# Optimization experiments

Measured on AMD Instinct MI355X. Metric: run time of the kernel, lower is better.

The kernel has to match this reference:

```python
import jax, jax.numpy as jnp
from jax import lax
import numpy as np

VOCAB, TAGS, EMBED, HIDDEN, BATCH, SEQ = 50000, 9, 300, 1000, 32, 200


def setup_inputs() -> dict:
    key = jax.random.key(0)
    ks = jax.random.split(key, 12)
    s_e = 1.0 / np.sqrt(HIDDEN)
    inp = {
        "x": jax.random.randint(ks[0], (SEQ, BATCH), 0, VOCAB),
        "y": jax.random.randint(ks[1], (SEQ, BATCH), 0, TAGS),
        "embed_w": jax.random.normal(ks[2], (VOCAB, EMBED), jnp.float32),
        "W_ih": jax.random.uniform(ks[3], (4 * HIDDEN, EMBED), jnp.float32, -s_e, s_e),
        "W_hh": jax.random.uniform(ks[4], (4 * HIDDEN, HIDDEN), jnp.float32, -s_e, s_e),
        "b_ih": jax.random.uniform(ks[5], (4 * HIDDEN,), jnp.float32, -s_e, s_e),
        "b_hh": jax.random.uniform(ks[6], (4 * HIDDEN,), jnp.float32, -s_e, s_e),
        "lin_w": jax.random.uniform(ks[7], (TAGS, HIDDEN), jnp.float32, -s_e, s_e),
        "lin_b": jax.random.uniform(ks[8], (TAGS,), jnp.float32, -s_e, s_e),
        "start_trans": jax.random.uniform(ks[9], (TAGS,), jnp.float32, -0.1, 0.1),
        "end_trans": jax.random.uniform(ks[10], (TAGS,), jnp.float32, -0.1, 0.1),
        "trans": jax.random.uniform(ks[11], (TAGS, TAGS), jnp.float32, -0.1, 0.1),
    }
    return inp


def _forward(x, y, embed_w, W_ih, W_hh, b_ih, b_hh, lin_w, lin_b, start_trans, end_trans, trans):
    T, B = x.shape
    H = W_hh.shape[1]
    embeds = embed_w[x]  # [T,B,E]
    # Precompute input contribution to gates: [T,B,4H]
    xg = jnp.einsum("tbe,ge->tbg", embeds, W_ih) + b_ih + b_hh

    def lstm_step(carry, xg_t):
        h, c = carry
        g = xg_t + h @ W_hh.T  # [B,4H]
        i, f, gg, o = jnp.split(g, 4, axis=-1)  # PyTorch gate order i,f,g,o
        c = jax.nn.sigmoid(f) * c + jax.nn.sigmoid(i) * jnp.tanh(gg)
        h = jax.nn.sigmoid(o) * jnp.tanh(c)
        return (h, c), h

    h0 = jnp.zeros((B, H), embeds.dtype)
    _, hs = lax.scan(lstm_step, (h0, h0), xg)  # hs: [T,B,H]

    tag_space = jnp.einsum("tbh,kh->tbk", hs, lin_w) + lin_b  # [T,B,K]
    # Faithful to original: log_softmax over dim=1 (the batch axis)
    emissions = jax.nn.log_softmax(tag_space, axis=1)

    # ---- CRF log-likelihood (pytorch-crf semantics, full mask, sum reduction) ----
    b_idx = jnp.arange(B)
    em_at_y = jnp.take_along_axis(emissions, y[:, :, None], axis=2)[:, :, 0]  # [T,B]
    numerator = (
        start_trans[y[0]]
        + em_at_y.sum(axis=0)
        + trans[y[:-1], y[1:]].sum(axis=0)
        + end_trans[y[-1]]
    )  # [B]

    alpha0 = start_trans[None, :] + emissions[0]  # [B,K]

    def crf_step(alpha, em_t):
        # alpha: [B,K] over previous tag; em_t: [B,K]
        nxt = jax.nn.logsumexp(alpha[:, :, None] + trans[None, :, :] + em_t[:, None, :], axis=1)
        return nxt, None

    alpha, _ = lax.scan(crf_step, alpha0, emissions[1:])
    log_z = jax.nn.logsumexp(alpha + end_trans[None, :], axis=1)  # [B]
    return (numerator - log_z).sum()


def reference(x, y, embed_w, W_ih, W_hh, b_ih, b_hh, lin_w, lin_b, start_trans, end_trans, trans):
    return _forward(x, y, embed_w, W_ih, W_hh, b_ih, b_hh, lin_w, lin_b, start_trans, end_trans, trans)
```

## Files before the change

kernel.cpp:

```cpp
#include <hip/hip_runtime.h>

#define T_SEQ 200
#define NB    32
#define NE    300
#define NH    1000
#define NK    9
#define NJ    4096
#define EPD   320
#define WSCALE 256.0f
#define HSCALE 16.0f
#define LSCALE 512.0f
#define GSCALE (1.0f / (256.0f * 16.0f))
#define TSCALE (1.0f / (16.0f * 512.0f))

typedef __attribute__((ext_vector_type(4))) float f32x4;
typedef __attribute__((ext_vector_type(8))) short s16x8;
typedef __attribute__((ext_vector_type(4))) short s16x4;
typedef unsigned long long u64;

__device__ __forceinline__ unsigned short f2bf(float f) {
    union { float f; unsigned u; } v; v.f = f;
    unsigned r = v.u + 0x7FFFu + ((v.u >> 16) & 1u);
    return (unsigned short)(r >> 16);
}
__device__ __forceinline__ float bf2f(unsigned short h) {
    union { unsigned u; float f; } v; v.u = ((unsigned)h) << 16;
    return v.f;
}
__device__ __forceinline__ float ftanh(float x) {
    float e = __expf(fminf(2.f * x, 80.f));
    return (e - 1.f) / (e + 1.f);
}
__device__ __forceinline__ float fsig(float x) {
    return 1.f / (1.f + __expf(-x));
}
__device__ __forceinline__ unsigned nt_poll(const unsigned* p) {
    unsigned r;
    asm volatile("global_load_dword %0, %1, off nt\n\t"
                 "s_waitcnt vmcnt(0)"
                 : "=v"(r) : "v"(p) : "memory");
    return r;
}
__device__ __forceinline__ void plain_pub(unsigned* p, unsigned v) {
    __hip_atomic_store(p, v, __ATOMIC_RELAXED, __HIP_MEMORY_SCOPE_WORKGROUP);
}

__global__ __launch_bounds__(256) void prep_emb(
    const int* __restrict__ x, const float* __restrict__ embed_w,
    unsigned short* __restrict__ emb_bf, unsigned* __restrict__ ctrl)
{
    const int t = blockIdx.x, tid = threadIdx.x;
    if (blockIdx.x == 0) {
        for (int i = tid; i < 2048; i += 256)
            ctrl[i] = (i == 497) ? 0xffffffffu : 0u;
    }
    for (int idx = tid; idx < NB * EPD; idx += 256) {
        int b = idx / EPD, e = idx - b * EPD;
        float v = (e < NE) ? embed_w[(size_t)x[t * NB + b] * NE + e] : 0.f;
        emb_bf[((size_t)t * NB + b) * EPD + e] = f2bf(v);
    }
}

__global__ __launch_bounds__(256) void prep_w(
    const float* __restrict__ W_ih, const float* __restrict__ b_ih,
    const float* __restrict__ b_hh, const float* __restrict__ lin_w,
    unsigned short* __restrict__ wih_bf, float* __restrict__ biasg,
    unsigned char* __restrict__ linw_q)
{
    const int blk = blockIdx.x, tid = threadIdx.x;
    for (int idx = tid; idx < 64 * EPD; idx += 256) {
        int jr = idx / EPD, e = idx - jr * EPD;
        int jp = blk * 64 + jr;
        int wgu = jp >> 7, rr = jp & 127, g = rr >> 5, uu = rr & 31;
        int m = wgu * 32 + uu;
        float v = (m < NH && e < NE) ? W_ih[(size_t)(g * NH + m) * NE + e] : 0.f;
        wih_bf[(size_t)jp * EPD + e] = f2bf(v);
    }
    if (tid < 64) {
        int jp = blk * 64 + tid;
        int wgu = jp >> 7, rr = jp & 127, g = rr >> 5, uu = rr & 31;
        int m = wgu * 32 + uu;
        biasg[jp] = (m < NH) ? (b_ih[g * NH + m] + b_hh[g * NH + m]) : 0.f;
    }
    if (blk < 16) {
        int n = blk, k = tid * 4;
        float v0 = (n < NK && k + 0 < NH) ? lin_w[(size_t)n * NH + k + 0] * LSCALE : 0.f;
        float v1 = (n < NK && k + 1 < NH) ? lin_w[(size_t)n * NH + k + 1] * LSCALE : 0.f;
        float v2 = (n < NK && k + 2 < NH) ? lin_w[(size_t)n * NH + k + 2] * LSCALE : 0.f;
        float v3 = (n < NK && k + 3 < NH) ? lin_w[(size_t)n * NH + k + 3] * LSCALE : 0.f;
        int p01 = __builtin_amdgcn_cvt_pk_fp8_f32(v0, v1, 0, false);
        int p23 = __builtin_amdgcn_cvt_pk_fp8_f32(v2, v3, 0, false);
        ((unsigned*)linw_q)[n * 256 + tid] =
            ((unsigned)p01 & 0xffffu) | ((unsigned)p23 << 16);
    }
}

__device__ __forceinline__ int gate_xg(unsigned* done, int ready, int tn, int lane) {
    while (ready <= tn) {
        unsigned v = 64u;
        if (lane < 8 && ready + lane < T_SEQ)
            v = __hip_atomic_load(&done[ready + lane], __ATOMIC_RELAXED,
                                  __HIP_MEMORY_SCOPE_AGENT);
        unsigned m = (unsigned)__ballot((int)(v >= 64u)) & 255u;
        if (m & 1u) {
            unsigned run = (m == 255u) ? 8u : (unsigned)__builtin_ctz(~m);
            ready += (int)run;
        } else {
            __builtin_amdgcn_s_sleep(1);
        }
    }
    return ready;
}

__global__ __launch_bounds__(256, 1) void lstm_kernel(
    const float* __restrict__ W_hh,
    const unsigned short* __restrict__ emb_bf,
    const unsigned short* __restrict__ wih_bf,
    const float* __restrict__ biasg,
    unsigned short* __restrict__ xg,
    unsigned char* __restrict__ h_q,
    unsigned* __restrict__ ctrl)
{
    __shared__ __align__(16) unsigned char s_w[128 * 1024];
    __shared__ int s_chunk, s_grp, s_pid, s_mode;

    const int tid = threadIdx.x;

    if (tid == 0) {
        unsigned xcc;
        asm volatile("s_getreg_b32 %0, hwreg(HW_REG_XCC_ID)" : "=s"(xcc));
        xcc &= 15u;
        unsigned myidx = __hip_atomic_fetch_add(&ctrl[480 + xcc], 1u,
                             __ATOMIC_RELAXED, __HIP_MEMORY_SCOPE_AGENT);
        __threadfence();
        unsigned tot = __hip_atomic_fetch_add(&ctrl[496], 1u,
                             __ATOMIC_RELAXED, __HIP_MEMORY_SCOPE_AGENT);
        if (tot == 255u) {
            __threadfence();
            unsigned w0 = 0xffu, w1 = 0xffu;
            for (unsigned xx = 0; xx < 16; ++xx) {
                unsigned cx = __hip_atomic_load(&ctrl[480 + xx], __ATOMIC_RELAXED,
                                                __HIP_MEMORY_SCOPE_AGENT);
                if (cx >= 32u) {
                    if (w0 == 0xffu) w0 = xx;
                    else { w1 = xx; break; }
                }
            }
            __hip_atomic_store(&ctrl[497], w0 | (w1 << 8), __ATOMIC_RELAXED,
                               __HIP_MEMORY_SCOPE_AGENT);
        }
        unsigned win;
        do {
            win = __hip_atomic_load(&ctrl[497], __ATOMIC_RELAXED,
                                    __HIP_MEMORY_SCOPE_AGENT);
        } while (win == 0xffffffffu);
        unsigned w0 = win & 0xffu, w1 = (win >> 8) & 0xffu;
        int grp = -1;
        if (xcc == w0 && myidx < 32u) grp = 0;
        else if (xcc == w1 && myidx < 32u) grp = 1;
        s_grp = grp;
        s_chunk = (grp >= 0) ? (int)myidx : -1;
        s_pid = (grp >= 0) ? -1
                     : (int)__hip_atomic_fetch_add(&ctrl[498], 1u,
                           __ATOMIC_RELAXED, __HIP_MEMORY_SCOPE_AGENT);
    }
    __syncthreads();
    const int chunk = s_chunk;
    const int w = tid >> 6, lane = tid & 63;
    const int col = lane & 15, quad = lane >> 4;
    unsigned* done = ctrl + 256;

    if (chunk < 0) {
        const int pid = s_pid;
        for (int g = pid; g < T_SEQ * 64; g += 192) {
            const int t = g >> 6, jt = g & 63;
            const unsigned short* eb = emb_bf + (size_t)t * NB * EPD;
            const unsigned short* wb = wih_bf + (size_t)(jt * 64 + w * 16 + col) * EPD;
            const unsigned short* ea0 = eb + (size_t)col * EPD;
            const unsigned short* ea1 = eb + (size_t)(16 + col) * EPD;

            f32x4 acc0 = {0.f, 0.f, 0.f, 0.f};
            f32x4 acc1 = {0.f, 0.f, 0.f, 0.f};
#pragma unroll
            for (int kc = 0; kc < EPD / 32; ++kc) {
                int ko = kc * 32 + quad * 8;
                s16x8 a0 = *(const s16x8*)&ea0[ko];
                s16x8 a1 = *(const s16x8*)&ea1[ko];
                s16x8 bb = *(const s16x8*)&wb[ko];
                acc0 = __builtin_amdgcn_mfma_f32_16x16x32_bf16(a0, bb, acc0, 0, 0, 0);
                acc1 = __builtin_amdgcn_mfma_f32_16x16x32_bf16(a1, bb, acc1, 0, 0, 0);
            }
            const int jp = jt * 64 + w * 16 + col;
            const float bi = biasg[jp];
            size_t base = ((size_t)t * NJ + jp) * NB;
            union { s16x4 v; u64 q; } p0, p1;
#pragma unroll
            for (int r = 0; r < 4; ++r) {
                p0.v[r] = (short)f2bf(acc0[r] + bi);
                p1.v[r] = (short)f2bf(acc1[r] + bi);
            }
            __hip_atomic_store((u64*)&xg[base + quad * 4], p0.q,
                               __ATOMIC_RELAXED, __HIP_MEMORY_SCOPE_AGENT);
            __hip_atomic_store((u64*)&xg[base + 16 + quad * 4], p1.q,
                               __ATOMIC_RELAXED, __HIP_MEMORY_SCOPE_AGENT);
            __syncthreads();
            if (tid == 0)
                __hip_atomic_fetch_add(&done[t], 1u, __ATOMIC_RELAXED,
                                       __HIP_MEMORY_SCOPE_AGENT);
        }
        return;
    }

    const int grp = s_grp;
    const size_t GOFF = (size_t)grp * 16384;
    unsigned* slowf = ctrl + grp * 64;
    unsigned* fastf = ctrl + 128 + grp * 64;
    unsigned* s_w32 = (unsigned*)s_w;

    for (int idx = tid; idx < 128 * 256; idx += 256) {
        int r = idx >> 8, dw = idx & 255;
        int g = r >> 5, uu = r & 31, m = chunk * 32 + uu;
        float4 w4 = make_float4(0.f, 0.f, 0.f, 0.f);
        if (m < NH && dw < 250)
            w4 = *(const float4*)&W_hh[(size_t)(g * NH + m) * NH + dw * 4];
        int p0 = __builtin_amdgcn_cvt_pk_fp8_f32(w4.x * WSCALE, w4.y * WSCALE, 0, false);
        int p1 = __builtin_amdgcn_cvt_pk_fp8_f32(w4.z * WSCALE, w4.w * WSCALE, 0, false);
        unsigned v = ((unsigned)p0 & 0xffffu) | ((unsigned)p1 << 16);
        int kb = dw >> 1;
        int kbs = kb ^ (r & 15);
        s_w32[r * 256 + (kbs << 1) + (dw & 1)] = v;
    }
    if (tid < 128)
        *(unsigned*)(h_q + GOFF + (size_t)chunk * 512 + tid * 4) = 0u;
    __syncthreads();
    if (tid == 0) {
        plain_pub(&fastf[chunk * 2 + 0], 1u);
        plain_pub(&fastf[chunk * 2 + 1], 1u);
        __hip_atomic_store(&slowf[chunk * 2 + 0], 1u, __ATOMIC_RELAXED,
                           __HIP_MEMORY_SCOPE_AGENT);
        __hip_atomic_store(&slowf[chunk * 2 + 1], 1u, __ATOMIC_RELAXED,
                           __HIP_MEMORY_SCOPE_AGENT);
    }
    if (grp == 0 && chunk == 0 && w == 0) {
        int md = 2;
        for (int it = 0; it < 8192; ++it) {
            unsigned v = nt_poll(&fastf[lane]);
            if (__all((int)(v >= 1u))) { md = 1; break; }
        }
        if (lane == 0) {
            __hip_atomic_store(&ctrl[499], (unsigned)md, __ATOMIC_RELAXED,
                               __HIP_MEMORY_SCOPE_AGENT);
            s_mode = md;
        }
    } else if (tid == 0) {
        unsigned m;
        do {
            m = __hip_atomic_load(&ctrl[499], __ATOMIC_RELAXED,
                                  __HIP_MEMORY_SCOPE_AGENT);
        } while (m == 0u);
        s_mode = (int)m;
    }
    __syncthreads();
    const int mode = s_mode;

    if (w >= 2) return;
    const int p = w;
    const int fid = chunk * 2 + w;

    int ready = gate_xg(done, 0, 1, lane);
    s16x4 xcur[4], xnxt[4];
#pragma unroll
    for (int g = 0; g < 4; ++g)
        xcur[g] = *(const s16x4*)&xg[((size_t)0 * NJ + chunk * 128 + (2 * g + p) * 16 + col) * NB
                                     + grp * 16 + quad * 4];

    float c[4] = {0.f, 0.f, 0.f, 0.f};
    const int rw = quad * 4;
    const int boff = col * 32 + quad * 8;

    for (int t = 0; t < T_SEQ; ++t) {
        const unsigned need = (unsigned)(t + 1);
        const int gt = t + 2;
        bool gate_pending = (gt < T_SEQ) && (ready <= gt);
        if (mode == 1) {
            for (;;) {
                unsigned v = nt_poll(&fastf[lane]);
                bool hok = __all((int)(v >= need));
                if (gate_pending) {
                    unsigned d = 64u;
                    if (lane < 8 && ready + lane < T_SEQ)
                        d = __hip_atomic_load(&done[ready + lane], __ATOMIC_RELAXED,
                                              __HIP_MEMORY_SCOPE_AGENT);
                    unsigned m = (unsigned)__ballot((int)(d >= 64u)) & 255u;
                    if (m & 1u)
                        ready += (m == 255u) ? 8 : (int)__builtin_ctz(~m);
                    gate_pending = (ready <= gt);
                }
                if (hok && !gate_pending) break;
            }
        } else {
            for (;;) {
                unsigned v = __hip_atomic_load(&slowf[lane], __ATOMIC_RELAXED,
                                               __HIP_MEMORY_SCOPE_AGENT);
                bool hok = __all((int)(v >= need));
                if (gate_pending) {
                    unsigned d = 64u;
                    if (lane < 8 && ready + lane < T_SEQ)
                        d = __hip_atomic_load(&done[ready + lane], __ATOMIC_RELAXED,
                                              __HIP_MEMORY_SCOPE_AGENT);
                    unsigned m = (unsigned)__ballot((int)(d >= 64u)) & 255u;
                    if (m & 1u)
                        ready += (m == 255u) ? 8 : (int)__builtin_ctz(~m);
                    gate_pending = (ready <= gt);
                }
                if (hok && !gate_pending) break;
            }
        }
        asm volatile("" ::: "memory");

        const unsigned char* pb = h_q + (size_t)t * 32768 + GOFF + boff;
        u64 a[32];
#pragma unroll
        for (int kc = 0; kc < 32; ++kc)
            a[kc] = *(const u64*)(pb + (size_t)kc * 512);

        if (t + 1 < T_SEQ) {
#pragma unroll
            for (int g = 0; g < 4; ++g)
                xnxt[g] = *(const s16x4*)&xg[((size_t)(t + 1) * NJ + chunk * 128 + (2 * g + p) * 16 + col) * NB
                                             + grp * 16 + quad * 4];
        }

        f32x4 acc0 = {0.f, 0.f, 0.f, 0.f};
        f32x4 acc1 = {0.f, 0.f, 0.f, 0.f};
        f32x4 acc2 = {0.f, 0.f, 0.f, 0.f};
        f32x4 acc3 = {0.f, 0.f, 0.f, 0.f};
#pragma unroll
        for (int kc = 0; kc < 32; ++kc) {
            int kb = kc * 4 + quad;
            u64 b0 = *(const u64*)&s_w[((0 * 2 + p) * 16 + col) * 1024 + ((kb ^ col) << 3)];
            u64 b1 = *(const u64*)&s_w[((1 * 2 + p) * 16 + col) * 1024 + ((kb ^ col) << 3)];
            u64 b2 = *(const u64*)&s_w[((2 * 2 + p) * 16 + col) * 1024 + ((kb ^ col) << 3)];
            u64 b3 = *(const u64*)&s_w[((3 * 2 + p) * 16 + col) * 1024 + ((kb ^ col) << 3)];
            acc0 = __builtin_amdgcn_mfma_f32_16x16x32_fp8_fp8((long)a[kc], (long)b0, acc0, 0, 0, 0);
            acc1 = __builtin_amdgcn_mfma_f32_16x16x32_fp8_fp8((long)a[kc], (long)b1, acc1, 0, 0, 0);
            acc2 = __builtin_amdgcn_mfma_f32_16x16x32_fp8_fp8((long)a[kc], (long)b2, acc2, 0, 0, 0);
            acc3 = __builtin_amdgcn_mfma_f32_16x16x32_fp8_fp8((long)a[kc], (long)b3, acc3, 0, 0, 0);
        }

        float hv[4];
#pragma unroll
        for (int r = 0; r < 4; ++r) {
            float gi = acc0[r] * GSCALE + bf2f((unsigned short)xcur[0][r]);
            float gf = acc1[r] * GSCALE + bf2f((unsigned short)xcur[1][r]);
            float gg = acc2[r] * GSCALE + bf2f((unsigned short)xcur[2][r]);
            float go = acc3[r] * GSCALE + bf2f((unsigned short)xcur[3][r]);
            c[r] = fsig(gf) * c[r] + fsig(gi) * ftanh(gg);
            hv[r] = fsig(go) * ftanh(c[r]);
        }
        {
            int p01 = __builtin_amdgcn_cvt_pk_fp8_f32(hv[0] * HSCALE, hv[1] * HSCALE, 0, false);
            int p23 = __builtin_amdgcn_cvt_pk_fp8_f32(hv[2] * HSCALE, hv[3] * HSCALE, 0, false);
            unsigned char* pg = h_q + (size_t)(t + 1) * 32768 + GOFF + (size_t)chunk * 512
                              + p * 16 + col;
            pg[(rw + 0) * 32] = (unsigned char)(p01 & 0xff);
            pg[(rw + 1) * 32] = (unsigned char)((p01 >> 8) & 0xff);
            pg[(rw + 2) * 32] = (unsigned char)(p23 & 0xff);
            pg[(rw + 3) * 32] = (unsigned char)((p23 >> 8) & 0xff);
        }
        asm volatile("s_waitcnt vmcnt(0)" ::: "memory");
        if (lane == 0) {
            plain_pub(&fastf[fid], (unsigned)(t + 2));
            if (mode == 2)
                __hip_atomic_store(&slowf[fid], (unsigned)(t + 2),
                                   __ATOMIC_RELAXED, __HIP_MEMORY_SCOPE_AGENT);
        }
#pragma unroll
        for (int g = 0; g < 4; ++g) xcur[g] = xnxt[g];
    }
}

__global__ __launch_bounds__(128) void tagem_kernel(
    const unsigned char* __restrict__ h_q,
    const unsigned char* __restrict__ linw_q,
    const float* __restrict__ lin_b,
    float* __restrict__ em)
{
    __shared__ float s_ts[NB * NK];
    __shared__ float s_lse[NK];
    const int t = blockIdx.x, tid = threadIdx.x;
    const int w = tid >> 6, lane = tid & 63;
    const int col = lane & 15, quad = lane >> 4;
    const unsigned char* pa = h_q + (size_t)(t + 1) * 32768 + (size_t)w * 16384
                            + col * 32 + quad * 8;
    const unsigned char* pw = linw_q + (size_t)col * 1024 + quad * 8;

    f32x4 acc = {0.f, 0.f, 0.f, 0.f};
#pragma unroll 8
    for (int kc = 0; kc < 32; ++kc) {
        u64 a  = *(const u64*)(pa + (size_t)kc * 512);
        u64 bv = *(const u64*)(pw + kc * 32);
        acc = __builtin_amdgcn_mfma_f32_16x16x32_fp8_fp8((long)a, (long)bv, acc, 0, 0, 0);
    }
    if (col < NK) {
        float lb = lin_b[col];
#pragma unroll
        for (int r = 0; r < 4; ++r)
            s_ts[(w * 16 + quad * 4 + r) * NK + col] = acc[r] * TSCALE + lb;
    }
    __syncthreads();
    if (tid < NK) {
        float m = -1e30f;
        for (int bb = 0; bb < NB; ++bb) m = fmaxf(m, s_ts[bb * NK + tid]);
        float s = 0.f;
        for (int bb = 0; bb < NB; ++bb) s += __expf(s_ts[bb * NK + tid] - m);
        s_lse[tid] = m + __logf(s);
    }
    __syncthreads();
    for (int idx = tid; idx < NB * NK; idx += 128) {
        int k = idx - (idx / NK) * NK;
        em[(size_t)t * NB * NK + idx] = s_ts[idx] - s_lse[k];
    }
}

__global__ __launch_bounds__(512) void crf_kernel(
    const int* __restrict__ y, const float* __restrict__ em,
    const float* __restrict__ start_trans, const float* __restrict__ end_trans,
    const float* __restrict__ trans, float* __restrict__ out)
{
    __shared__ float s_trans[NK * NK];
    __shared__ float s_red[NB];
    __shared__ int   s_y[T_SEQ * NB];
    const int tid = threadIdx.x;
    const int gb = tid >> 4;
    const int q  = tid & 15;
    const int lane = tid & 63;
    const int gbase = lane & 48;

    if (tid < NK * NK) s_trans[tid] = trans[tid];
    for (int i = tid; i < T_SEQ * NB; i += 512) s_y[i] = y[i];
    __syncthreads();

    float trC[NK];
#pragma unroll
    for (int i = 0; i < NK; ++i)
        trC[i] = (q < NK) ? s_trans[i * NK + q] : 0.f;

    float emv0 = (q < NK) ? em[gb * NK + q] : -1e30f;
    int yp = s_y[gb];
    float num = start_trans[yp] + __shfl(emv0, gbase | yp, 64);
    float alpha = (q < NK) ? (start_trans[q] + emv0) : -1e30f;

    float e[8];
#pragma unroll
    for (int j = 0; j < 8; ++j) {
        int t = 1 + j;
        e[j] = (q < NK && t < T_SEQ) ? em[(size_t)(t * NB + gb) * NK + q] : -1e30f;
    }
    for (int blk = 0; blk < 25; ++blk) {
        float enx[8];
        const int tb = 1 + (blk + 1) * 8;
#pragma unroll
        for (int j = 0; j < 8; ++j) {
            int t = tb + j;
            enx[j] = (q < NK && t < T_SEQ) ? em[(size_t)(t * NB + gb) * NK + q] : -1e30f;
        }
#pragma unroll
        for (int j = 0; j < 8; ++j) {
            int t = 1 + blk * 8 + j;
            if (t < T_SEQ) {
                float ev = e[j];
                int yc = s_y[t * NB + gb];
                num += s_trans[yp * NK + yc] + __shfl(ev, gbase | yc, 64);
                yp = yc;
                float a_i[NK];
#pragma unroll
                for (int i = 0; i < NK; ++i)
                    a_i[i] = __shfl(alpha, gbase | i, 64) + trC[i];
                float m = a_i[0];
#pragma unroll
                for (int i = 1; i < NK; ++i) m = fmaxf(m, a_i[i]);
                float s = 0.f;
#pragma unroll
                for (int i = 0; i < NK; ++i) s += __expf(a_i[i] - m);
                alpha = (q < NK) ? (ev + m + __logf(s)) : -1e30f;
            }
        }
#pragma unroll
        for (int j = 0; j < 8; ++j) e[j] = enx[j];
    }

    num += end_trans[yp];
    float v = (q < NK) ? (alpha + end_trans[q]) : -1e30f;
    float mg = v;
#pragma unroll
    for (int off = 8; off >= 1; off >>= 1)
        mg = fmaxf(mg, __shfl_xor(mg, off, 64));
    float sg = __expf(v - mg);
#pragma unroll
    for (int off = 8; off >= 1; off >>= 1)
        sg += __shfl_xor(sg, off, 64);
    float lz = mg + __logf(sg);
    if (q == 0) s_red[gb] = num - lz;
    __syncthreads();
    if (tid == 0) {
        float tot = 0.f;
        for (int i = 0; i < NB; ++i) tot += s_red[i];
        out[0] = tot;
    }
}

extern "C" void kernel_launch(void* const* d_in, const int* in_sizes, int n_in,
                              void* d_out, int out_size, void* d_ws, size_t ws_size,
                              hipStream_t stream)
{
    const int*   x           = (const int*)d_in[0];
    const int*   y           = (const int*)d_in[1];
    const float* embed_w     = (const float*)d_in[2];
    const float* W_ih        = (const float*)d_in[3];
    const float* W_hh        = (const float*)d_in[4];
    const float* b_ih        = (const float*)d_in[5];
    const float* b_hh        = (const float*)d_in[6];
    const float* lin_w       = (const float*)d_in[7];
    const float* lin_b       = (const float*)d_in[8];
    const float* start_trans = (const float*)d_in[9];
    const float* end_trans   = (const float*)d_in[10];
    const float* trans       = (const float*)d_in[11];
    float* out = (float*)d_out;

    char* ws = (char*)d_ws;
    unsigned short* xg     = (unsigned short*)(ws);
    unsigned char*  h_q    = (unsigned char*)(ws + 52428800);
    unsigned char*  linw_q = (unsigned char*)(ws + 59015168);
    float*          em     = (float*)(ws + 65601536);
    unsigned*       ctrl   = (unsigned*)(ws + 65831936);
    float*          biasg  = (float*)(ws + 65840128);
    unsigned short* emb_bf = (unsigned short*)(ws + 65856512);
    unsigned short* wih_bf = (unsigned short*)(ws + 69952512);

    prep_emb<<<dim3(T_SEQ), 256, 0, stream>>>(x, embed_w, emb_bf, ctrl);
    prep_w<<<dim3(64), 256, 0, stream>>>(W_ih, b_ih, b_hh, lin_w, wih_bf, biasg, linw_q);

    lstm_kernel<<<dim3(256), 256, 0, stream>>>(W_hh, emb_bf, wih_bf, biasg,
                                               xg, h_q, ctrl);

    tagem_kernel<<<dim3(T_SEQ), 128, 0, stream>>>(h_q, linw_q, lin_b, em);
    crf_kernel<<<dim3(1), 512, 0, stream>>>(y, em, start_trans, end_trans, trans, out);
}
```

Measured before the change: 983.5 us.

## Offload flag polling to helper waves and merge prep kernels

Two otherwise idle waves per workgroup now do all global polling. One tracks the per-chunk h-ready flags, the other tracks the xg-done counters, and each relays progress through shared-memory variables that the two compute waves spin on. This takes global-memory polling latency off the recurrent critical path. The next-step xg load now happens after the h store and before the publish, and the publish waits with a partial vmcnt. The two prep kernels are also fused into one launch. The risks are the looser waitcnt ordering between the stores and the flag publish, and extra wave activity on the CU.

```diff
diff --git a/kernel.cpp b/kernel.cpp
--- a/kernel.cpp
+++ b/kernel.cpp
@@ -45,45 +45,45 @@
     __hip_atomic_store(p, v, __ATOMIC_RELAXED, __HIP_MEMORY_SCOPE_WORKGROUP);
 }
 
-__global__ __launch_bounds__(256) void prep_emb(
+__global__ __launch_bounds__(256) void prep_all(
     const int* __restrict__ x, const float* __restrict__ embed_w,
-    unsigned short* __restrict__ emb_bf, unsigned* __restrict__ ctrl)
-{
-    const int t = blockIdx.x, tid = threadIdx.x;
-    if (blockIdx.x == 0) {
-        for (int i = tid; i < 2048; i += 256)
-            ctrl[i] = (i == 497) ? 0xffffffffu : 0u;
-    }
-    for (int idx = tid; idx < NB * EPD; idx += 256) {
-        int b = idx / EPD, e = idx - b * EPD;
-        float v = (e < NE) ? embed_w[(size_t)x[t * NB + b] * NE + e] : 0.f;
-        emb_bf[((size_t)t * NB + b) * EPD + e] = f2bf(v);
-    }
-}
-
-__global__ __launch_bounds__(256) void prep_w(
     const float* __restrict__ W_ih, const float* __restrict__ b_ih,
     const float* __restrict__ b_hh, const float* __restrict__ lin_w,
-    unsigned short* __restrict__ wih_bf, float* __restrict__ biasg,
-    unsigned char* __restrict__ linw_q)
+    unsigned short* __restrict__ emb_bf, unsigned short* __restrict__ wih_bf,
+    float* __restrict__ biasg, unsigned char* __restrict__ linw_q,
+    unsigned* __restrict__ ctrl)
 {
     const int blk = blockIdx.x, tid = threadIdx.x;
+    if (blk < T_SEQ) {
+        const int t = blk;
+        if (blk == 0) {
+            for (int i = tid; i < 2048; i += 256)
+                ctrl[i] = (i == 497) ? 0xffffffffu : 0u;
+        }
+        for (int idx = tid; idx < NB * EPD; idx += 256) {
+            int b = idx / EPD, e = idx - b * EPD;
+            float v = (e < NE) ? embed_w[(size_t)x[t * NB + b] * NE + e] : 0.f;
+            emb_bf[((size_t)t * NB + b) * EPD + e] = f2bf(v);
+        }
+        return;
+    }
+    const int b2 = blk - T_SEQ;
     for (int idx = tid; idx < 64 * EPD; idx += 256) {
         int jr = idx / EPD, e = idx - jr * EPD;
-        int jp = blk * 64 + jr;
+        int jp = b2 * 64 + jr;
         int wgu = jp >> 7, rr = jp & 127, g = rr >> 5, uu = rr & 31;
         int m = wgu * 32 + uu;
         float v = (m < NH && e < NE) ? W_ih[(size_t)(g * NH + m) * NE + e] : 0.f;
         wih_bf[(size_t)jp * EPD + e] = f2bf(v);
     }
     if (tid < 64) {
-        int jp = blk * 64 + tid;
+        int jp = b2 * 64 + tid;
         int wgu = jp >> 7, rr = jp & 127, g = rr >> 5, uu = rr & 31;
         int m = wgu * 32 + uu;
         biasg[jp] = (m < NH) ? (b_ih[g * NH + m] + b_hh[g * NH + m]) : 0.f;
     }
-    if (blk < 16) {
-        int n = blk, k = tid * 4;
+    if (b2 < 16) {
+        int n = b2, k = tid * 4;
         float v0 = (n < NK && k + 0 < NH) ? lin_w[(size_t)n * NH + k + 0] * LSCALE : 0.f;
         float v1 = (n < NK && k + 1 < NH) ? lin_w[(size_t)n * NH + k + 1] * LSCALE : 0.f;
         float v2 = (n < NK && k + 2 < NH) ? lin_w[(size_t)n * NH + k + 2] * LSCALE : 0.f;
@@ -93,23 +93,6 @@
         ((unsigned*)linw_q)[n * 256 + tid] =
             ((unsigned)p01 & 0xffffu) | ((unsigned)p23 << 16);
     }
-}
-
-__device__ __forceinline__ int gate_xg(unsigned* done, int ready, int tn, int lane) {
-    while (ready <= tn) {
-        unsigned v = 64u;
-        if (lane < 8 && ready + lane < T_SEQ)
-            v = __hip_atomic_load(&done[ready + lane], __ATOMIC_RELAXED,
-                                  __HIP_MEMORY_SCOPE_AGENT);
-        unsigned m = (unsigned)__ballot((int)(v >= 64u)) & 255u;
-        if (m & 1u) {
-            unsigned run = (m == 255u) ? 8u : (unsigned)__builtin_ctz(~m);
-            ready += (int)run;
-        } else {
-            __builtin_amdgcn_s_sleep(1);
-        }
-    }
-    return ready;
 }
 
 __global__ __launch_bounds__(256, 1) void lstm_kernel(
@@ -123,10 +106,12 @@
 {
     __shared__ __align__(16) unsigned char s_w[128 * 1024];
     __shared__ int s_chunk, s_grp, s_pid, s_mode;
+    __shared__ int s_go, s_ready;
 
     const int tid = threadIdx.x;
 
     if (tid == 0) {
+        s_go = 0; s_ready = 0;
         unsigned xcc;
         asm volatile("s_getreg_b32 %0, hwreg(HW_REG_XCC_ID)" : "=s"(xcc));
         xcc &= 15u;
@@ -263,59 +248,58 @@
     __syncthreads();
     const int mode = s_mode;
 
-    if (w >= 2) return;
+    volatile int* vgo = (volatile int*)&s_go;
+    volatile int* vready = (volatile int*)&s_ready;
+
+    if (w == 2) {
+        int need = 1;
+        while (need <= T_SEQ) {
+            unsigned v;
+            if (mode == 1) v = nt_poll(&fastf[lane]);
+            else v = __hip_atomic_load(&slowf[lane], __ATOMIC_RELAXED,
+                                       __HIP_MEMORY_SCOPE_AGENT);
+            while (need <= T_SEQ && __all((int)(v >= (unsigned)need))) {
+                if (lane == 0) *vgo = need;
+                ++need;
+            }
+        }
+        return;
+    }
+    if (w == 3) {
+        int ready = 0;
+        while (ready < T_SEQ) {
+            unsigned v = 64u;
+            if (lane < 8 && ready + lane < T_SEQ)
+                v = __hip_atomic_load(&done[ready + lane], __ATOMIC_RELAXED,
+                                      __HIP_MEMORY_SCOPE_AGENT);
+            unsigned m = (unsigned)__ballot((int)(v >= 64u)) & 255u;
+            if (m & 1u) {
+                ready += (m == 255u) ? 8 : (int)__builtin_ctz(~m);
+                if (lane == 0) *vready = ready;
+            } else {
+                __builtin_amdgcn_s_sleep(1);
+            }
+        }
+        return;
+    }
+
     const int p = w;
     const int fid = chunk * 2 + w;
 
-    int ready = gate_xg(done, 0, 1, lane);
-    s16x4 xcur[4], xnxt[4];
+    while (*vready < 1) { }
+    asm volatile("" ::: "memory");
+    s16x4 xA[4], xB[4];
 #pragma unroll
     for (int g = 0; g < 4; ++g)
-        xcur[g] = *(const s16x4*)&xg[((size_t)0 * NJ + chunk * 128 + (2 * g + p) * 16 + col) * NB
-                                     + grp * 16 + quad * 4];
+        xA[g] = *(const s16x4*)&xg[((size_t)0 * NJ + chunk * 128 + (2 * g + p) * 16 + col) * NB
+                                   + grp * 16 + quad * 4];
 
     float c[4] = {0.f, 0.f, 0.f, 0.f};
     const int rw = quad * 4;
     const int boff = col * 32 + quad * 8;
 
-    for (int t = 0; t < T_SEQ; ++t) {
-        const unsigned need = (unsigned)(t + 1);
-        const int gt = t + 2;
-        bool gate_pending = (gt < T_SEQ) && (ready <= gt);
-        if (mode == 1) {
-            for (;;) {
-                unsigned v = nt_poll(&fastf[lane]);
-                bool hok = __all((int)(v >= need));
-                if (gate_pending) {
-                    unsigned d = 64u;
-                    if (lane < 8 && ready + lane < T_SEQ)
-                        d = __hip_atomic_load(&done[ready + lane], __ATOMIC_RELAXED,
-                                              __HIP_MEMORY_SCOPE_AGENT);
-                    unsigned m = (unsigned)__ballot((int)(d >= 64u)) & 255u;
-                    if (m & 1u)
-                        ready += (m == 255u) ? 8 : (int)__builtin_ctz(~m);
-                    gate_pending = (ready <= gt);
-                }
-                if (hok && !gate_pending) break;
-            }
-        } else {
-            for (;;) {
-                unsigned v = __hip_atomic_load(&slowf[lane], __ATOMIC_RELAXED,
-                                               __HIP_MEMORY_SCOPE_AGENT);
-                bool hok = __all((int)(v >= need));
-                if (gate_pending) {
-                    unsigned d = 64u;
-                    if (lane < 8 && ready + lane < T_SEQ)
-                        d = __hip_atomic_load(&done[ready + lane], __ATOMIC_RELAXED,
-                                              __HIP_MEMORY_SCOPE_AGENT);
-                    unsigned m = (unsigned)__ballot((int)(d >= 64u)) & 255u;
-                    if (m & 1u)
-                        ready += (m == 255u) ? 8 : (int)__builtin_ctz(~m);
-                    gate_pending = (ready <= gt);
-                }
-                if (hok && !gate_pending) break;
-            }
-        }
+    auto step = [&](int t, s16x4 (&xin)[4], s16x4 (&xout)[4]) {
+        while (*vgo < t + 1) { }
         asm volatile("" ::: "memory");
 
         const unsigned char* pb = h_q + (size_t)t * 32768 + GOFF + boff;
@@ -323,13 +307,6 @@
 #pragma unroll
         for (int kc = 0; kc < 32; ++kc)
             a[kc] = *(const u64*)(pb + (size_t)kc * 512);
-
-        if (t + 1 < T_SEQ) {
-#pragma unroll
-            for (int g = 0; g < 4; ++g)
-                xnxt[g] = *(const s16x4*)&xg[((size_t)(t + 1) * NJ + chunk * 128 + (2 * g + p) * 16 + col) * NB
-                                             + grp * 16 + quad * 4];
-        }
 
         f32x4 acc0 = {0.f, 0.f, 0.f, 0.f};
         f32x4 acc1 = {0.f, 0.f, 0.f, 0.f};
@@ -351,10 +328,10 @@
         float hv[4];
 #pragma unroll
         for (int r = 0; r < 4; ++r) {
-            float gi = acc0[r] * GSCALE + bf2f((unsigned short)xcur[0][r]);
-            float gf = acc1[r] * GSCALE + bf2f((unsigned short)xcur[1][r]);
-            float gg = acc2[r] * GSCALE + bf2f((unsigned short)xcur[2][r]);
-            float go = acc3[r] * GSCALE + bf2f((unsigned short)xcur[3][r]);
+            float gi = acc0[r] * GSCALE + bf2f((unsigned short)xin[0][r]);
+            float gf = acc1[r] * GSCALE + bf2f((unsigned short)xin[1][r]);
+            float gg = acc2[r] * GSCALE + bf2f((unsigned short)xin[2][r]);
+            float go = acc3[r] * GSCALE + bf2f((unsigned short)xin[3][r]);
             c[r] = fsig(gf) * c[r] + fsig(gi) * ftanh(gg);
             hv[r] = fsig(go) * ftanh(c[r]);
         }
@@ -368,15 +345,29 @@
             pg[(rw + 2) * 32] = (unsigned char)(p23 & 0xff);
             pg[(rw + 3) * 32] = (unsigned char)((p23 >> 8) & 0xff);
         }
-        asm volatile("s_waitcnt vmcnt(0)" ::: "memory");
-        if (lane == 0) {
-            plain_pub(&fastf[fid], (unsigned)(t + 2));
-            if (mode == 2)
-                __hip_atomic_store(&slowf[fid], (unsigned)(t + 2),
-                                   __ATOMIC_RELAXED, __HIP_MEMORY_SCOPE_AGENT);
-        }
-#pragma unroll
-        for (int g = 0; g < 4; ++g) xcur[g] = xnxt[g];
+        asm volatile("" ::: "memory");
+
+        if (t + 1 < T_SEQ) {
+            while (*vready < t + 2) { }
+            asm volatile("" ::: "memory");
+#pragma unroll
+            for (int g = 0; g < 4; ++g)
+                xout[g] = *(const s16x4*)&xg[((size_t)(t + 1) * NJ + chunk * 128 + (2 * g + p) * 16 + col) * NB
+                                             + grp * 16 + quad * 4];
+            asm volatile("" ::: "memory");
+            asm volatile("s_waitcnt vmcnt(4)" ::: "memory");
+            if (lane == 0) {
+                plain_pub(&fastf[fid], (unsigned)(t + 2));
+                if (mode == 2)
+                    __hip_atomic_store(&slowf[fid], (unsigned)(t + 2),
+                                       __ATOMIC_RELAXED, __HIP_MEMORY_SCOPE_AGENT);
+            }
+        }
+    };
+
+    for (int tt = 0; tt < T_SEQ; tt += 2) {
+        step(tt + 0, xA, xB);
+        step(tt + 1, xB, xA);
     }
 }
 
@@ -538,8 +529,9 @@
     unsigned short* emb_bf = (unsigned short*)(ws + 65856512);
     unsigned short* wih_bf = (unsigned short*)(ws + 69952512);
 
-    prep_emb<<<dim3(T_SEQ), 256, 0, stream>>>(x, embed_w, emb_bf, ctrl);
-    prep_w<<<dim3(64), 256, 0, stream>>>(W_ih, b_ih, b_hh, lin_w, wih_bf, biasg, linw_q);
+    prep_all<<<dim3(T_SEQ + 64), 256, 0, stream>>>(x, embed_w, W_ih, b_ih, b_hh,
+                                                   lin_w, emb_bf, wih_bf, biasg,
+                                                   linw_q, ctrl);
 
     lstm_kernel<<<dim3(256), 256, 0, stream>>>(W_hh, emb_bf, wih_bf, biasg,
                                                xg, h_q, ctrl);
```

After: 1.290 ms. 31.2% more time.

## Merge prep kernels, fuse tag emission with CRF via flags, relax LSTM publish wait

Applied to the files above, without the earlier changes.

Combines the two prep kernels into one launch, and merges the tag-emission and CRF kernels into a single grid. In the merged grid the CRF block polls per-timestep flags so it can start consuming emissions while other blocks are still producing them. In the LSTM loop, the next step's xg prefetch is now issued before the h-publish flag, and the wait before publishing is vmcnt(4) instead of vmcnt(0), so the prefetch loads stay in flight. The loop is also unrolled by two with ping-pong buffers. The changes aim to cut launch overhead and shorten the critical path of the recurrence. The risk is that the CRF block spin-waits if it is scheduled before the producer blocks, and that the relaxed wait count depends on the exact order of outstanding memory operations.

```diff
diff --git a/kernel.cpp b/kernel.cpp
--- a/kernel.cpp
+++ b/kernel.cpp
@@ -45,45 +45,45 @@
     __hip_atomic_store(p, v, __ATOMIC_RELAXED, __HIP_MEMORY_SCOPE_WORKGROUP);
 }
 
-__global__ __launch_bounds__(256) void prep_emb(
+__global__ __launch_bounds__(256) void prep_all(
     const int* __restrict__ x, const float* __restrict__ embed_w,
-    unsigned short* __restrict__ emb_bf, unsigned* __restrict__ ctrl)
-{
-    const int t = blockIdx.x, tid = threadIdx.x;
-    if (blockIdx.x == 0) {
-        for (int i = tid; i < 2048; i += 256)
-            ctrl[i] = (i == 497) ? 0xffffffffu : 0u;
-    }
-    for (int idx = tid; idx < NB * EPD; idx += 256) {
-        int b = idx / EPD, e = idx - b * EPD;
-        float v = (e < NE) ? embed_w[(size_t)x[t * NB + b] * NE + e] : 0.f;
-        emb_bf[((size_t)t * NB + b) * EPD + e] = f2bf(v);
-    }
-}
-
-__global__ __launch_bounds__(256) void prep_w(
     const float* __restrict__ W_ih, const float* __restrict__ b_ih,
     const float* __restrict__ b_hh, const float* __restrict__ lin_w,
-    unsigned short* __restrict__ wih_bf, float* __restrict__ biasg,
-    unsigned char* __restrict__ linw_q)
+    unsigned short* __restrict__ emb_bf, unsigned short* __restrict__ wih_bf,
+    float* __restrict__ biasg, unsigned char* __restrict__ linw_q,
+    unsigned* __restrict__ ctrl)
 {
     const int blk = blockIdx.x, tid = threadIdx.x;
+    if (blk < T_SEQ) {
+        const int t = blk;
+        if (blk == 0) {
+            for (int i = tid; i < 2048; i += 256)
+                ctrl[i] = (i == 497) ? 0xffffffffu : 0u;
+        }
+        for (int idx = tid; idx < NB * EPD; idx += 256) {
+            int b = idx / EPD, e = idx - b * EPD;
+            float v = (e < NE) ? embed_w[(size_t)x[t * NB + b] * NE + e] : 0.f;
+            emb_bf[((size_t)t * NB + b) * EPD + e] = f2bf(v);
+        }
+        return;
+    }
+    const int b2 = blk - T_SEQ;
     for (int idx = tid; idx < 64 * EPD; idx += 256) {
         int jr = idx / EPD, e = idx - jr * EPD;
-        int jp = blk * 64 + jr;
+        int jp = b2 * 64 + jr;
         int wgu = jp >> 7, rr = jp & 127, g = rr >> 5, uu = rr & 31;
         int m = wgu * 32 + uu;
         float v = (m < NH && e < NE) ? W_ih[(size_t)(g * NH + m) * NE + e] : 0.f;
         wih_bf[(size_t)jp * EPD + e] = f2bf(v);
     }
     if (tid < 64) {
-        int jp = blk * 64 + tid;
+        int jp = b2 * 64 + tid;
         int wgu = jp >> 7, rr = jp & 127, g = rr >> 5, uu = rr & 31;
         int m = wgu * 32 + uu;
         biasg[jp] = (m < NH) ? (b_ih[g * NH + m] + b_hh[g * NH + m]) : 0.f;
     }
-    if (blk < 16) {
-        int n = blk, k = tid * 4;
+    if (b2 < 16) {
+        int n = b2, k = tid * 4;
         float v0 = (n < NK && k + 0 < NH) ? lin_w[(size_t)n * NH + k + 0] * LSCALE : 0.f;
         float v1 = (n < NK && k + 1 < NH) ? lin_w[(size_t)n * NH + k + 1] * LSCALE : 0.f;
         float v2 = (n < NK && k + 2 < NH) ? lin_w[(size_t)n * NH + k + 2] * LSCALE : 0.f;
@@ -268,17 +268,17 @@
     const int fid = chunk * 2 + w;
 
     int ready = gate_xg(done, 0, 1, lane);
-    s16x4 xcur[4], xnxt[4];
+    s16x4 xA[4], xB[4];
 #pragma unroll
     for (int g = 0; g < 4; ++g)
-        xcur[g] = *(const s16x4*)&xg[((size_t)0 * NJ + chunk * 128 + (2 * g + p) * 16 + col) * NB
-                                     + grp * 16 + quad * 4];
+        xA[g] = *(const s16x4*)&xg[((size_t)0 * NJ + chunk * 128 + (2 * g + p) * 16 + col) * NB
+                                   + grp * 16 + quad * 4];
 
     float c[4] = {0.f, 0.f, 0.f, 0.f};
     const int rw = quad * 4;
     const int boff = col * 32 + quad * 8;
 
-    for (int t = 0; t < T_SEQ; ++t) {
+    auto step = [&](int t, s16x4 (&xin)[4], s16x4 (&xout)[4]) {
         const unsigned need = (unsigned)(t + 1);
         const int gt = t + 2;
         bool gate_pending = (gt < T_SEQ) && (ready <= gt);
@@ -324,13 +324,6 @@
         for (int kc = 0; kc < 32; ++kc)
             a[kc] = *(const u64*)(pb + (size_t)kc * 512);
 
-        if (t + 1 < T_SEQ) {
-#pragma unroll
-            for (int g = 0; g < 4; ++g)
-                xnxt[g] = *(const s16x4*)&xg[((size_t)(t + 1) * NJ + chunk * 128 + (2 * g + p) * 16 + col) * NB
-                                             + grp * 16 + quad * 4];
-        }
-
         f32x4 acc0 = {0.f, 0.f, 0.f, 0.f};
         f32x4 acc1 = {0.f, 0.f, 0.f, 0.f};
         f32x4 acc2 = {0.f, 0.f, 0.f, 0.f};
@@ -351,10 +344,10 @@
         float hv[4];
 #pragma unroll
         for (int r = 0; r < 4; ++r) {
-            float gi = acc0[r] * GSCALE + bf2f((unsigned short)xcur[0][r]);
-            float gf = acc1[r] * GSCALE + bf2f((unsigned short)xcur[1][r]);
-            float gg = acc2[r] * GSCALE + bf2f((unsigned short)xcur[2][r]);
-            float go = acc3[r] * GSCALE + bf2f((unsigned short)xcur[3][r]);
+            float gi = acc0[r] * GSCALE + bf2f((unsigned short)xin[0][r]);
+            float gf = acc1[r] * GSCALE + bf2f((unsigned short)xin[1][r]);
+            float gg = acc2[r] * GSCALE + bf2f((unsigned short)xin[2][r]);
+            float go = acc3[r] * GSCALE + bf2f((unsigned short)xin[3][r]);
             c[r] = fsig(gf) * c[r] + fsig(gi) * ftanh(gg);
             hv[r] = fsig(go) * ftanh(c[r]);
         }
@@ -368,70 +361,96 @@
             pg[(rw + 2) * 32] = (unsigned char)(p23 & 0xff);
             pg[(rw + 3) * 32] = (unsigned char)((p23 >> 8) & 0xff);
         }
-        asm volatile("s_waitcnt vmcnt(0)" ::: "memory");
-        if (lane == 0) {
-            plain_pub(&fastf[fid], (unsigned)(t + 2));
-            if (mode == 2)
-                __hip_atomic_store(&slowf[fid], (unsigned)(t + 2),
-                                   __ATOMIC_RELAXED, __HIP_MEMORY_SCOPE_AGENT);
-        }
-#pragma unroll
-        for (int g = 0; g < 4; ++g) xcur[g] = xnxt[g];
-    }
-}
-
-__global__ __launch_bounds__(128) void tagem_kernel(
+        asm volatile("" ::: "memory");
+
+        if (t + 1 < T_SEQ) {
+#pragma unroll
+            for (int g = 0; g < 4; ++g)
+                xout[g] = *(const s16x4*)&xg[((size_t)(t + 1) * NJ + chunk * 128 + (2 * g + p) * 16 + col) * NB
+                                             + grp * 16 + quad * 4];
+            asm volatile("" ::: "memory");
+            asm volatile("s_waitcnt vmcnt(4)" ::: "memory");
+            if (lane == 0) {
+                plain_pub(&fastf[fid], (unsigned)(t + 2));
+                if (mode == 2)
+                    __hip_atomic_store(&slowf[fid], (unsigned)(t + 2),
+                                       __ATOMIC_RELAXED, __HIP_MEMORY_SCOPE_AGENT);
+            }
+        }
+    };
+
+    for (int tt = 0; tt < T_SEQ; tt += 2) {
+        step(tt + 0, xA, xB);
+        step(tt + 1, xB, xA);
+    }
+}
+
+__global__ __launch_bounds__(512) void tagem_crf(
     const unsigned char* __restrict__ h_q,
     const unsigned char* __restrict__ linw_q,
     const float* __restrict__ lin_b,
-    float* __restrict__ em)
+    const int* __restrict__ y,
+    const float* __restrict__ start_trans, const float* __restrict__ end_trans,
+    const float* __restrict__ trans,
+    float* __restrict__ em, unsigned* __restrict__ ctrl,
+    float* __restrict__ out)
 {
     __shared__ float s_ts[NB * NK];
     __shared__ float s_lse[NK];
-    const int t = blockIdx.x, tid = threadIdx.x;
-    const int w = tid >> 6, lane = tid & 63;
-    const int col = lane & 15, quad = lane >> 4;
-    const unsigned char* pa = h_q + (size_t)(t + 1) * 32768 + (size_t)w * 16384
-                            + col * 32 + quad * 8;
-    const unsigned char* pw = linw_q + (size_t)col * 1024 + quad * 8;
-
-    f32x4 acc = {0.f, 0.f, 0.f, 0.f};
-#pragma unroll 8
-    for (int kc = 0; kc < 32; ++kc) {
-        u64 a  = *(const u64*)(pa + (size_t)kc * 512);
-        u64 bv = *(const u64*)(pw + kc * 32);
-        acc = __builtin_amdgcn_mfma_f32_16x16x32_fp8_fp8((long)a, (long)bv, acc, 0, 0, 0);
-    }
-    if (col < NK) {
-        float lb = lin_b[col];
-#pragma unroll
-        for (int r = 0; r < 4; ++r)
-            s_ts[(w * 16 + quad * 4 + r) * NK + col] = acc[r] * TSCALE + lb;
-    }
-    __syncthreads();
-    if (tid < NK) {
-        float m = -1e30f;
-        for (int bb = 0; bb < NB; ++bb) m = fmaxf(m, s_ts[bb * NK + tid]);
-        float s = 0.f;
-        for (int bb = 0; bb < NB; ++bb) s += __expf(s_ts[bb * NK + tid] - m);
-        s_lse[tid] = m + __logf(s);
-    }
-    __syncthreads();
-    for (int idx = tid; idx < NB * NK; idx += 128) {
-        int k = idx - (idx / NK) * NK;
-        em[(size_t)t * NB * NK + idx] = s_ts[idx] - s_lse[k];
-    }
-}
-
-__global__ __launch_bounds__(512) void crf_kernel(
-    const int* __restrict__ y, const float* __restrict__ em,
-    const float* __restrict__ start_trans, const float* __restrict__ end_trans,
-    const float* __restrict__ trans, float* __restrict__ out)
-{
     __shared__ float s_trans[NK * NK];
     __shared__ float s_red[NB];
     __shared__ int   s_y[T_SEQ * NB];
-    const int tid = threadIdx.x;
+    const int blk = blockIdx.x, tid = threadIdx.x;
+    unsigned* pflag = ctrl + 512;
+
+    if (blk < T_SEQ) {
+        const int t = blk;
+        const int w = tid >> 6, lane = tid & 63;
+        const int col = lane & 15, quad = lane >> 4;
+        if (w < 2) {
+            const unsigned char* pa = h_q + (size_t)(t + 1) * 32768 + (size_t)w * 16384
+                                    + col * 32 + quad * 8;
+            const unsigned char* pw = linw_q + (size_t)col * 1024 + quad * 8;
+            f32x4 acc = {0.f, 0.f, 0.f, 0.f};
+#pragma unroll 8
+            for (int kc = 0; kc < 32; ++kc) {
+                u64 a  = *(const u64*)(pa + (size_t)kc * 512);
+                u64 bv = *(const u64*)(pw + kc * 32);
+                acc = __builtin_amdgcn_mfma_f32_16x16x32_fp8_fp8((long)a, (long)bv, acc, 0, 0, 0);
+            }
+            if (col < NK) {
+                float lb = lin_b[col];
+#pragma unroll
+                for (int r = 0; r < 4; ++r)
+                    s_ts[(w * 16 + quad * 4 + r) * NK + col] = acc[r] * TSCALE + lb;
+            }
+        }
+        __syncthreads();
+        if (tid < NK) {
+            float m = -1e30f;
+            for (int bb = 0; bb < NB; ++bb) m = fmaxf(m, s_ts[bb * NK + tid]);
+            float s = 0.f;
+            for (int bb = 0; bb < NB; ++bb) s += __expf(s_ts[bb * NK + tid] - m);
+            s_lse[tid] = m + __logf(s);
+        }
+        __syncthreads();
+        if (tid < NB * NK) {
+            int k = tid - (tid / NK) * NK;
+            union { float f; unsigned u; } cv;
+            cv.f = s_ts[tid] - s_lse[k];
+            __hip_atomic_store((unsigned*)em + (size_t)t * NB * NK + tid, cv.u,
+                               __ATOMIC_RELAXED, __HIP_MEMORY_SCOPE_AGENT);
+        }
+        asm volatile("s_waitcnt vmcnt(0)" ::: "memory");
+        __syncthreads();
+        if (tid == 0) {
+            __threadfence();
+            __hip_atomic_store(&pflag[t], 1u, __ATOMIC_RELAXED,
+                               __HIP_MEMORY_SCOPE_AGENT);
+        }
+        return;
+    }
+
     const int gb = tid >> 4;
     const int q  = tid & 15;
     const int lane = tid & 63;
@@ -441,12 +460,32 @@
     for (int i = tid; i < T_SEQ * NB; i += 512) s_y[i] = y[i];
     __syncthreads();
 
+    auto wait_pages = [&](int base) {
+        for (;;) {
+            unsigned v = 1u;
+            if (lane < 8 && base + lane < T_SEQ)
+                v = __hip_atomic_load(&pflag[base + lane], __ATOMIC_RELAXED,
+                                      __HIP_MEMORY_SCOPE_AGENT);
+            if (__all((int)(v >= 1u))) break;
+            __builtin_amdgcn_s_sleep(2);
+        }
+    };
+    auto emload = [&](int t) -> float {
+        union { unsigned u; float f; } cv;
+        cv.u = __hip_atomic_load((const unsigned*)em + (size_t)(t * NB + gb) * NK + q,
+                                 __ATOMIC_RELAXED, __HIP_MEMORY_SCOPE_AGENT);
+        return cv.f;
+    };
+
     float trC[NK];
 #pragma unroll
     for (int i = 0; i < NK; ++i)
         trC[i] = (q < NK) ? s_trans[i * NK + q] : 0.f;
 
-    float emv0 = (q < NK) ? em[gb * NK + q] : -1e30f;
+    wait_pages(0);
+    wait_pages(8);
+
+    float emv0 = (q < NK) ? emload(0) : -1e30f;
     int yp = s_y[gb];
     float num = start_trans[yp] + __shfl(emv0, gbase | yp, 64);
     float alpha = (q < NK) ? (start_trans[q] + emv0) : -1e30f;
@@ -455,19 +494,20 @@
 #pragma unroll
     for (int j = 0; j < 8; ++j) {
         int t = 1 + j;
-        e[j] = (q < NK && t < T_SEQ) ? em[(size_t)(t * NB + gb) * NK + q] : -1e30f;
-    }
-    for (int blk = 0; blk < 25; ++blk) {
+        e[j] = (q < NK && t < T_SEQ) ? emload(t) : -1e30f;
+    }
+    for (int blk2 = 0; blk2 < 25; ++blk2) {
         float enx[8];
-        const int tb = 1 + (blk + 1) * 8;
+        const int tb = 1 + (blk2 + 1) * 8;
+        wait_pages(tb);
 #pragma unroll
         for (int j = 0; j < 8; ++j) {
             int t = tb + j;
-            enx[j] = (q < NK && t < T_SEQ) ? em[(size_t)(t * NB + gb) * NK + q] : -1e30f;
+            enx[j] = (q < NK && t < T_SEQ) ? emload(t) : -1e30f;
         }
 #pragma unroll
         for (int j = 0; j < 8; ++j) {
-            int t = 1 + blk * 8 + j;
+            int t = 1 + blk2 * 8 + j;
             if (t < T_SEQ) {
                 float ev = e[j];
                 int yc = s_y[t * NB + gb];
@@ -538,12 +578,14 @@
     unsigned short* emb_bf = (unsigned short*)(ws + 65856512);
     unsigned short* wih_bf = (unsigned short*)(ws + 69952512);
 
-    prep_emb<<<dim3(T_SEQ), 256, 0, stream>>>(x, embed_w, emb_bf, ctrl);
-    prep_w<<<dim3(64), 256, 0, stream>>>(W_ih, b_ih, b_hh, lin_w, wih_bf, biasg, linw_q);
+    prep_all<<<dim3(T_SEQ + 64), 256, 0, stream>>>(x, embed_w, W_ih, b_ih, b_hh,
+                                                   lin_w, emb_bf, wih_bf, biasg,
+                                                   linw_q, ctrl);
 
     lstm_kernel<<<dim3(256), 256, 0, stream>>>(W_hh, emb_bf, wih_bf, biasg,
                                                xg, h_q, ctrl);
 
-    tagem_kernel<<<dim3(T_SEQ), 128, 0, stream>>>(h_q, linw_q, lin_b, em);
-    crf_kernel<<<dim3(1), 512, 0, stream>>>(y, em, start_trans, end_trans, trans, out);
-}
+    tagem_crf<<<dim3(T_SEQ + 1), 512, 0, stream>>>(h_q, linw_q, lin_b, y,
+                                                   start_trans, end_trans, trans,
+                                                   em, ctrl, out);
+}
```

Measured after the change: 1.136 ms. +15.5%, slower.
